# Kernel optimization log

Hardware: AMD Instinct MI355X
Metric: run time of the kernel (lower is better)

## Reference

```python
import jax, jax.numpy as jnp
import numpy as np

H, C, PQ, PV = 12, 16, 4, 8   # heads, c_hidden, qk points, v points
CS, CZ = 384, 128
INF, EPS = 1e5, 1e-8


def quat_to_rot(q):
    w, x, y, z = q[..., 0], q[..., 1], q[..., 2], q[..., 3]
    r = jnp.stack([
        1 - 2 * (y * y + z * z), 2 * (x * y - w * z), 2 * (x * z + w * y),
        2 * (x * y + w * z), 1 - 2 * (x * x + z * z), 2 * (y * z - w * x),
        2 * (x * z - w * y), 2 * (y * z + w * x), 1 - 2 * (x * x + y * y)],
        axis=-1)
    return r.reshape(q.shape[:-1] + (3, 3))


def setup_inputs() -> dict:
    key = jax.random.key(0)
    ks = jax.random.split(key, 20)
    B, N = 1, 768
    s = jax.random.normal(ks[0], (B, N, CS), jnp.float32)
    z = jax.random.normal(ks[1], (B, N, N, CZ), jnp.float32)
    quat = jax.random.normal(ks[2], (B, N, 4), jnp.float32)
    quat = quat / jnp.linalg.norm(quat, axis=-1, keepdims=True)
    rot = quat_to_rot(quat)
    trans = 10.0 * jax.random.normal(ks[3], (B, N, 3), jnp.float32)
    mask = jnp.ones((B, N), jnp.float32)
    ss = jax.random.uniform(ks[4], (B, N, N), jnp.float32)
    sc = 0.02
    W_q = sc * jax.random.normal(ks[5], (CS, H * C), jnp.float32)
    b_q = jnp.zeros((H * C,), jnp.float32)
    W_kv = sc * jax.random.normal(ks[6], (CS, 2 * H * C), jnp.float32)
    b_kv = jnp.zeros((2 * H * C,), jnp.float32)
    W_qp = sc * jax.random.normal(ks[7], (CS, H * PQ * 3), jnp.float32)
    b_qp = jnp.zeros((H * PQ * 3,), jnp.float32)
    W_kvp = sc * jax.random.normal(ks[8], (CS, H * (PQ + PV) * 3), jnp.float32)
    b_kvp = jnp.zeros((H * (PQ + PV) * 3,), jnp.float32)
    W_b = sc * jax.random.normal(ks[9], (CZ, H), jnp.float32)
    b_b = jnp.zeros((H,), jnp.float32)
    head_weights = 0.1 * jax.random.normal(ks[10], (H,), jnp.float32)
    cdim = H * (CZ + C + PV * 4)
    W_out = sc * jax.random.normal(ks[11], (cdim, CS), jnp.float32)
    b_out = jnp.zeros((CS,), jnp.float32)
    return dict(s=s, z=z, rot=rot, trans=trans, mask=mask, ss=ss,
                W_q=W_q, b_q=b_q, W_kv=W_kv, b_kv=b_kv, W_qp=W_qp, b_qp=b_qp,
                W_kvp=W_kvp, b_kvp=b_kvp, W_b=W_b, b_b=b_b,
                head_weights=head_weights, W_out=W_out, b_out=b_out)


def reference(s, z, rot, trans, mask, ss, W_q, b_q, W_kv, b_kv, W_qp, b_qp,
              W_kvp, b_kvp, W_b, b_b, head_weights, W_out, b_out):
    B, N, _ = s.shape
    # scalar q/k/v  [B,N,H,C]
    q = (s @ W_q + b_q).reshape(B, N, H, C)
    kv = (s @ W_kv + b_kv).reshape(B, N, H, 2 * C)
    k, v = kv[..., :C], kv[..., C:]
    # point q/k/v: linear output is [x_all, y_all, z_all] -> stack on last dim
    qp = s @ W_qp + b_qp                                  # [B,N,H*PQ*3]
    qp = jnp.stack(jnp.split(qp, 3, axis=-1), axis=-1)    # [B,N,H*PQ,3] local
    qp = jnp.einsum('bnxy,bnpy->bnpx', rot, qp) + trans[:, :, None]
    qp = qp.reshape(B, N, H, PQ, 3)                       # global frame
    kvp = s @ W_kvp + b_kvp
    kvp = jnp.stack(jnp.split(kvp, 3, axis=-1), axis=-1)  # [B,N,H*(PQ+PV),3]
    kvp = jnp.einsum('bnxy,bnpy->bnpx', rot, kvp) + trans[:, :, None]
    kvp = kvp.reshape(B, N, H, PQ + PV, 3)
    kp, vp = kvp[..., :PQ, :], kvp[..., PQ:, :]
    # scalar attention logits + pair bias
    b = z @ W_b + b_b                                     # [B,N,N,H]
    a = jnp.einsum('bihc,bjhc->bhij', q, k) * np.sqrt(1.0 / (3 * C))
    a = a + np.sqrt(1.0 / 3) * jnp.transpose(b, (0, 3, 1, 2))
    # point-distance attention
    diff = qp[:, :, None] - kp[:, None]                   # [B,N,N,H,PQ,3]
    d2 = jnp.sum(diff * diff, axis=-1)                    # [B,N,N,H,PQ]
    hw = jax.nn.softplus(head_weights) * np.sqrt(1.0 / (3 * (PQ * 9.0 / 2)))
    pt = -0.5 * jnp.sum(d2 * hw[None, None, None, :, None], axis=-1)  # [B,N,N,H]
    a = a + jnp.transpose(pt, (0, 3, 1, 2))
    sq_mask = INF * (mask[:, :, None] * mask[:, None, :] - 1.0)
    a = a + sq_mask[:, None]
    # weighted softmax (ss_usage='multiply', t_ss=1): weights = exp(ss) - 0.99
    weights = jnp.exp(ss) - 0.99                          # [B,N,N]
    e = jnp.exp(a - jnp.max(a, axis=-1, keepdims=True))
    we = e * weights[:, None]
    a = we / jnp.sum(we, axis=-1, keepdims=True)          # [B,H,N,N]
    # outputs
    o = jnp.einsum('bhij,bjhc->bihc', a, v).reshape(B, N, H * C)
    o_pt = jnp.einsum('bhij,bjhpc->bihpc', a, vp)         # [B,N,H,PV,3] global
    o_pt = jnp.einsum('bnyx,bnhpy->bnhpx', rot, o_pt - trans[:, :, None, None])
    o_pt_norm = jnp.sqrt(jnp.sum(o_pt ** 2, axis=-1) + EPS).reshape(B, N, H * PV)
    o_pt = o_pt.reshape(B, N, H * PV, 3)
    o_pair = jnp.einsum('bhij,bijc->bihc', a, z).reshape(B, N, H * CZ)
    cat = jnp.concatenate(
        [o, o_pt[..., 0], o_pt[..., 1], o_pt[..., 2], o_pt_norm, o_pair], axis=-1)
    return cat @ W_out + b_out
```

## Files before the change

### kernel.cpp

```cpp
#include <hip/hip_runtime.h>
#include <math.h>

#define NN 768
#define CSD 384
#define HD 12
#define CD 16
#define PQD 4
#define PVD 8
#define CZD 128
#define CATD 2112

#define OFF_Q      0u
#define OFF_K      147456u
#define OFF_V      294912u
#define OFF_QP     442368u
#define OFF_KP     552960u
#define OFF_VP     663552u
#define OFF_RAW    884736u
#define OFF_B      1327104u
#define OFF_A      8404992u
#define OFF_CAT    15482880u

__device__ __forceinline__ float wcol_val(const float* Wq, const float* Wkv,
                                          const float* Wqp, const float* Wkvp,
                                          int k, int col) {
  if (col < 192) return Wq[k*192 + col];
  if (col < 576) return Wkv[k*384 + (col-192)];
  if (col < 720) return Wqp[k*144 + (col-576)];
  return Wkvp[k*432 + (col-720)];
}
__device__ __forceinline__ float bias_val(const float* bq, const float* bkv,
                                          const float* bqp, const float* bkvp, int col) {
  if (col < 192) return bq[col];
  if (col < 576) return bkv[col-192];
  if (col < 720) return bqp[col-576];
  return bkvp[col-720];
}

__global__ __launch_bounds__(256) void k_proj(const float* __restrict__ s,
    const float* __restrict__ Wq, const float* __restrict__ bq,
    const float* __restrict__ Wkv, const float* __restrict__ bkv,
    const float* __restrict__ Wqp, const float* __restrict__ bqp,
    const float* __restrict__ Wkvp, const float* __restrict__ bkvp,
    float* __restrict__ ws) {
  __shared__ float At[64*17];
  __shared__ float Bt[16*64];
  int t = threadIdx.x;
  int c0 = blockIdx.x * 64;
  int r0 = blockIdx.y * 64;
  float acc[4][4] = {};
  int cc = t & 15, rr = t >> 4;
  for (int kt = 0; kt < CSD; kt += 16) {
    int ka = t & 15, mb = t >> 4;
#pragma unroll
    for (int p = 0; p < 4; ++p) {
      int m = mb + p*16;
      At[m*17 + ka] = s[(r0+m)*CSD + kt + ka];
    }
    int cb = t & 63, kb = t >> 6;
#pragma unroll
    for (int p = 0; p < 4; ++p) {
      int kk = kb + p*4;
      Bt[kk*64 + cb] = wcol_val(Wq,Wkv,Wqp,Wkvp, kt+kk, c0+cb);
    }
    __syncthreads();
#pragma unroll
    for (int k = 0; k < 16; ++k) {
      float a0 = At[(rr*4+0)*17 + k];
      float a1 = At[(rr*4+1)*17 + k];
      float a2 = At[(rr*4+2)*17 + k];
      float a3 = At[(rr*4+3)*17 + k];
      float4 b4 = *(const float4*)&Bt[k*64 + cc*4];
      acc[0][0] = fmaf(a0,b4.x,acc[0][0]); acc[0][1] = fmaf(a0,b4.y,acc[0][1]);
      acc[0][2] = fmaf(a0,b4.z,acc[0][2]); acc[0][3] = fmaf(a0,b4.w,acc[0][3]);
      acc[1][0] = fmaf(a1,b4.x,acc[1][0]); acc[1][1] = fmaf(a1,b4.y,acc[1][1]);
      acc[1][2] = fmaf(a1,b4.z,acc[1][2]); acc[1][3] = fmaf(a1,b4.w,acc[1][3]);
      acc[2][0] = fmaf(a2,b4.x,acc[2][0]); acc[2][1] = fmaf(a2,b4.y,acc[2][1]);
      acc[2][2] = fmaf(a2,b4.z,acc[2][2]); acc[2][3] = fmaf(a2,b4.w,acc[2][3]);
      acc[3][0] = fmaf(a3,b4.x,acc[3][0]); acc[3][1] = fmaf(a3,b4.y,acc[3][1]);
      acc[3][2] = fmaf(a3,b4.z,acc[3][2]); acc[3][3] = fmaf(a3,b4.w,acc[3][3]);
    }
    __syncthreads();
  }
  float* qbuf = ws + OFF_Q; float* kbuf = ws + OFF_K; float* vbuf = ws + OFF_V;
  float* raw  = ws + OFF_RAW;
#pragma unroll
  for (int jj = 0; jj < 4; ++jj) {
    int col = c0 + cc*4 + jj;
    float bv = bias_val(bq,bkv,bqp,bkvp,col);
#pragma unroll
    for (int ii = 0; ii < 4; ++ii) {
      int row = r0 + rr*4 + ii;
      float val = acc[ii][jj] + bv;
      if (col < 192) {
        int h = col >> 4, c = col & 15;
        qbuf[(h*NN + row)*CD + c] = val;
      } else if (col < 576) {
        int u = col - 192; int h = u >> 5; int c2 = u & 31;
        if (c2 < 16) kbuf[(h*NN+row)*CD + c2] = val;
        else         vbuf[(h*NN+row)*CD + (c2-16)] = val;
      } else {
        raw[row*576 + (col-576)] = val;
      }
    }
  }
}

__global__ __launch_bounds__(256) void k_points(const float* __restrict__ rot,
    const float* __restrict__ trans, float* __restrict__ ws) {
  int tg = blockIdx.x*256 + threadIdx.x;
  int n = tg / 192, pidx = tg % 192;
  const float* raw = ws + OFF_RAW + n*576;
  float v0, v1, v2;
  if (pidx < 48) { v0 = raw[pidx]; v1 = raw[48+pidx]; v2 = raw[96+pidx]; }
  else { int pp = pidx-48; v0 = raw[144+pp]; v1 = raw[288+pp]; v2 = raw[432+pp]; }
  const float* R = rot + n*9; const float* T = trans + n*3;
  float g0 = R[0]*v0 + R[1]*v1 + R[2]*v2 + T[0];
  float g1 = R[3]*v0 + R[4]*v1 + R[5]*v2 + T[1];
  float g2 = R[6]*v0 + R[7]*v1 + R[8]*v2 + T[2];
  if (pidx < 48) {
    int h = pidx >> 2, p = pidx & 3;
    float* qp = ws + OFF_QP + ((h*NN + n)*PQD + p)*3;
    qp[0]=g0; qp[1]=g1; qp[2]=g2;
  } else {
    int pp = pidx - 48; int h = pp/12; int q12 = pp - 12*h;
    if (q12 < 4) { float* kp = ws + OFF_KP + ((h*NN+n)*PQD + q12)*3; kp[0]=g0; kp[1]=g1; kp[2]=g2; }
    else         { float* vp = ws + OFF_VP + ((h*NN+n)*PVD + (q12-4))*3; vp[0]=g0; vp[1]=g1; vp[2]=g2; }
  }
}

__global__ __launch_bounds__(256) void k_bias(const float* __restrict__ z,
    const float* __restrict__ Wb, const float* __restrict__ bb, float* __restrict__ ws) {
  __shared__ float wb_sm[CZD*HD];
  __shared__ float bb_sm[HD];
  int t = threadIdx.x;
  for (int idx = t; idx < CZD*HD; idx += 256) wb_sm[idx] = Wb[idx];
  if (t < HD) bb_sm[t] = bb[t];
  __syncthreads();

  int w = t >> 6, lane = t & 63;
  int i = blockIdx.x*4 + w;
  int j = blockIdx.y*64 + lane;
  const float* zrow = z + ((size_t)i*NN + j)*CZD;
  float acc[12];
#pragma unroll
  for (int h = 0; h < 12; ++h) acc[h] = 0.f;

  for (int c0 = 0; c0 < CZD; c0 += 32) {
    float4 zr[8];
#pragma unroll
    for (int u = 0; u < 8; ++u)
      zr[u] = *(const float4*)(zrow + c0 + 4*u);
#pragma unroll
    for (int u = 0; u < 8; ++u) {
#pragma unroll
      for (int cc = 0; cc < 4; ++cc) {
        int c = c0 + 4*u + cc;
        float zv = (cc==0) ? zr[u].x : (cc==1) ? zr[u].y : (cc==2) ? zr[u].z : zr[u].w;
        float4 w0 = *(const float4*)&wb_sm[c*12];
        float4 w1 = *(const float4*)&wb_sm[c*12 + 4];
        float4 w2 = *(const float4*)&wb_sm[c*12 + 8];
        acc[0] = fmaf(zv, w0.x, acc[0]); acc[1] = fmaf(zv, w0.y, acc[1]);
        acc[2] = fmaf(zv, w0.z, acc[2]); acc[3] = fmaf(zv, w0.w, acc[3]);
        acc[4] = fmaf(zv, w1.x, acc[4]); acc[5] = fmaf(zv, w1.y, acc[5]);
        acc[6] = fmaf(zv, w1.z, acc[6]); acc[7] = fmaf(zv, w1.w, acc[7]);
        acc[8] = fmaf(zv, w2.x, acc[8]); acc[9] = fmaf(zv, w2.y, acc[9]);
        acc[10] = fmaf(zv, w2.z, acc[10]); acc[11] = fmaf(zv, w2.w, acc[11]);
      }
    }
  }
  float* bmat = ws + OFF_B;
  const float s2 = 0.57735026918962576f;
#pragma unroll
  for (int h = 0; h < 12; ++h)
    bmat[((size_t)i*HD + h)*NN + j] = s2*(acc[h] + bb_sm[h]);
}

__global__ __launch_bounds__(256) void k_attn(
    const float* __restrict__ mask, const float* __restrict__ ss,
    const float* __restrict__ hwts, float* __restrict__ ws) {
  int h = blockIdx.x, i = blockIdx.y;
  int t = threadIdx.x;
  __shared__ float qsm[16];
  __shared__ float qpsm[12];
  __shared__ float wred[8];
  const float* qbuf = ws + OFF_Q; const float* kbuf = ws + OFF_K;
  const float* qp   = ws + OFF_QP; const float* kp  = ws + OFF_KP;
  const float* bmat = ws + OFF_B;
  float* abuf = ws + OFF_A;
  if (t < 16) qsm[t] = qbuf[(h*NN+i)*CD + t];
  else if (t < 28) qpsm[t-16] = qp[(h*NN+i)*12 + (t-16)];
  __syncthreads();
  float coef = -0.5f * 0.13608276348795434f * log1pf(__expf(hwts[h]));
  float mi = mask[i];
  const float s1 = 0.14433756729740643f;
  float l3[3], ss3[3];
#pragma unroll
  for (int jj = 0; jj < 3; ++jj) {
    int j = t + jj*256;
    const float4* kb = (const float4*)(kbuf + (h*NN+j)*CD);
    float dot = 0.f;
#pragma unroll
    for (int u = 0; u < 4; ++u) {
      float4 kv = kb[u];
      dot = fmaf(qsm[u*4+0], kv.x, dot);
      dot = fmaf(qsm[u*4+1], kv.y, dot);
      dot = fmaf(qsm[u*4+2], kv.z, dot);
      dot = fmaf(qsm[u*4+3], kv.w, dot);
    }
    const float4* kpb = (const float4*)(kp + (h*NN+j)*12);
    float pts = 0.f;
#pragma unroll
    for (int u = 0; u < 3; ++u) {
      float4 kpv = kpb[u];
      float d;
      d = qpsm[u*4+0]-kpv.x; pts = fmaf(d,d,pts);
      d = qpsm[u*4+1]-kpv.y; pts = fmaf(d,d,pts);
      d = qpsm[u*4+2]-kpv.z; pts = fmaf(d,d,pts);
      d = qpsm[u*4+3]-kpv.w; pts = fmaf(d,d,pts);
    }
    float bterm = bmat[((size_t)i*HD + h)*NN + j];
    float lg = fmaf(dot, s1, bterm) + coef*pts + 100000.0f*(mi*mask[j] - 1.0f);
    l3[jj] = lg; ss3[jj] = ss[i*NN + j];
  }
  float mx = fmaxf(l3[0], fmaxf(l3[1], l3[2]));
#pragma unroll
  for (int off = 32; off >= 1; off >>= 1) mx = fmaxf(mx, __shfl_xor(mx, off));
  if ((t & 63) == 0) wred[t>>6] = mx;
  __syncthreads();
  mx = fmaxf(fmaxf(wred[0],wred[1]), fmaxf(wred[2],wred[3]));
  float e3[3]; float sum = 0.f;
#pragma unroll
  for (int jj = 0; jj < 3; ++jj) {
    e3[jj] = __expf(l3[jj]-mx) * (__expf(ss3[jj]) - 0.99f);
    sum += e3[jj];
  }
#pragma unroll
  for (int off = 32; off >= 1; off >>= 1) sum += __shfl_xor(sum, off);
  if ((t & 63) == 0) wred[4 + (t>>6)] = sum;
  __syncthreads();
  sum = (wred[4]+wred[5]) + (wred[6]+wred[7]);
  float inv = 1.0f / sum;
#pragma unroll
  for (int jj = 0; jj < 3; ++jj)
    abuf[((size_t)h*NN + i)*NN + t + jj*256] = e3[jj]*inv;
}

__global__ __launch_bounds__(256) void k_out_v(
    const float* __restrict__ rot, const float* __restrict__ trans, float* __restrict__ ws) {
  int h = blockIdx.x;
  int i = blockIdx.y*4 + (threadIdx.x >> 6);
  int lane = threadIdx.x & 63;
  const float* abuf = ws + OFF_A; const float* vbuf = ws + OFF_V; const float* vpbuf = ws + OFF_VP;
  float* cat = ws + OFF_CAT;
  const float* arow = abuf + ((size_t)h*NN + i)*NN;
  float acc = 0.f;
  if (lane < 40) {
    const float* ptr; int stride;
    if (lane < 16) { ptr = vbuf + (size_t)(h*NN)*CD + lane; stride = CD; }
    else           { ptr = vpbuf + (size_t)(h*NN)*24 + (lane-16); stride = 24; }
    for (int j = 0; j < NN; j += 4) {
      float4 a4 = *(const float4*)(arow + j);
      float x0 = ptr[0];
      float x1 = ptr[stride];
      float x2 = ptr[2*stride];
      float x3 = ptr[3*stride];
      ptr += 4*stride;
      acc = fmaf(a4.x, x0, acc);
      acc = fmaf(a4.y, x1, acc);
      acc = fmaf(a4.z, x2, acc);
      acc = fmaf(a4.w, x3, acc);
    }
  }
  if (lane < 16) {
    cat[(size_t)i*CATD + h*CD + lane] = acc;
  } else if (lane < 40) {
    int pv = lane - 16; int p = pv/3; int x = pv - 3*p;
    int base = 16 + p*3;
    float g0 = __shfl(acc, base+0);
    float g1 = __shfl(acc, base+1);
    float g2 = __shfl(acc, base+2);
    float v0 = g0 - trans[i*3+0];
    float v1 = g1 - trans[i*3+1];
    float v2 = g2 - trans[i*3+2];
    float loc = rot[i*9 + 0*3 + x]*v0 + rot[i*9 + 1*3 + x]*v1 + rot[i*9 + 2*3 + x]*v2;
    cat[(size_t)i*CATD + 192 + x*96 + h*PVD + p] = loc;
    float sq = loc*loc;
    float n2 = __shfl(sq, base+0) + __shfl(sq, base+1) + __shfl(sq, base+2);
    if (x == 0) cat[(size_t)i*CATD + 480 + h*PVD + p] = sqrtf(n2 + 1e-8f);
  }
}

__global__ __launch_bounds__(256) void k_out_pair(const float* __restrict__ z, float* __restrict__ ws) {
  __shared__ float a_sm[HD*NN];
  __shared__ float4 psm[4][HD][32];
  int i = blockIdx.x;
  int t = threadIdx.x;
  const float* abuf = ws + OFF_A;
  float* cat = ws + OFF_CAT;
  for (int h = 0; h < HD; ++h) {
    if (t < 192)
      *(float4*)&a_sm[h*NN + t*4] = *(const float4*)(abuf + ((size_t)h*NN + i)*NN + t*4);
  }
  __syncthreads();
  int c4 = t & 31, jc = t >> 5;
  const float* zbase = z + ((size_t)i*NN + (size_t)jc*96)*CZD + c4*4;
  float4 acc[12];
#pragma unroll
  for (int h = 0; h < 12; ++h) acc[h] = make_float4(0.f,0.f,0.f,0.f);
  for (int jj = 0; jj < 96; jj += 4) {
    float4 z0 = *(const float4*)(zbase + (size_t)(jj+0)*CZD);
    float4 z1 = *(const float4*)(zbase + (size_t)(jj+1)*CZD);
    float4 z2 = *(const float4*)(zbase + (size_t)(jj+2)*CZD);
    float4 z3 = *(const float4*)(zbase + (size_t)(jj+3)*CZD);
    int j0 = jc*96 + jj;
#pragma unroll
    for (int h = 0; h < 12; ++h) {
      float4 av = *(const float4*)&a_sm[h*NN + j0];
      acc[h].x = fmaf(av.x, z0.x, acc[h].x); acc[h].y = fmaf(av.x, z0.y, acc[h].y);
      acc[h].z = fmaf(av.x, z0.z, acc[h].z); acc[h].w = fmaf(av.x, z0.w, acc[h].w);
      acc[h].x = fmaf(av.y, z1.x, acc[h].x); acc[h].y = fmaf(av.y, z1.y, acc[h].y);
      acc[h].z = fmaf(av.y, z1.z, acc[h].z); acc[h].w = fmaf(av.y, z1.w, acc[h].w);
      acc[h].x = fmaf(av.z, z2.x, acc[h].x); acc[h].y = fmaf(av.z, z2.y, acc[h].y);
      acc[h].z = fmaf(av.z, z2.z, acc[h].z); acc[h].w = fmaf(av.z, z2.w, acc[h].w);
      acc[h].x = fmaf(av.w, z3.x, acc[h].x); acc[h].y = fmaf(av.w, z3.y, acc[h].y);
      acc[h].z = fmaf(av.w, z3.z, acc[h].z); acc[h].w = fmaf(av.w, z3.w, acc[h].w);
    }
  }
  int wv = t >> 6, ln = t & 63;
#pragma unroll
  for (int h = 0; h < 12; ++h) {
    acc[h].x += __shfl_down(acc[h].x, 32);
    acc[h].y += __shfl_down(acc[h].y, 32);
    acc[h].z += __shfl_down(acc[h].z, 32);
    acc[h].w += __shfl_down(acc[h].w, 32);
  }
  if (ln < 32) {
#pragma unroll
    for (int h = 0; h < 12; ++h) psm[wv][h][ln] = acc[h];
  }
  __syncthreads();
  for (int o = t; o < 384; o += 256) {
    int h = o >> 5, cc = o & 31;
    float4 s0 = psm[0][h][cc], s1 = psm[1][h][cc], s2 = psm[2][h][cc], s3 = psm[3][h][cc];
    float4 r;
    r.x = (s0.x+s1.x)+(s2.x+s3.x);
    r.y = (s0.y+s1.y)+(s2.y+s3.y);
    r.z = (s0.z+s1.z)+(s2.z+s3.z);
    r.w = (s0.w+s1.w)+(s2.w+s3.w);
    *(float4*)&cat[(size_t)i*CATD + 576 + h*CZD + cc*4] = r;
  }
}

__global__ __launch_bounds__(256) void k_init_out(const float* __restrict__ bout, float* __restrict__ out) {
  int idx = blockIdx.x*256 + threadIdx.x;
  if (idx < NN*CSD) out[idx] = bout[idx % CSD];
}

__global__ __launch_bounds__(256) void k_final(const float* __restrict__ Wout,
    float* __restrict__ out, const float* __restrict__ ws) {
  __shared__ float At[64*17];
  __shared__ float Bt[16*64];
  const float* cat = ws + OFF_CAT;
  int t = threadIdx.x;
  int c0 = blockIdx.x*64, r0 = blockIdx.y*64;
  int kstart = blockIdx.z*528;
  float acc[4][4] = {};
  int cc = t & 15, rr = t >> 4;
  for (int kt = 0; kt < 528; kt += 16) {
    int ka = t & 15, mb = t >> 4;
#pragma unroll
    for (int p = 0; p < 4; ++p) {
      int m = mb + p*16;
      At[m*17 + ka] = cat[(size_t)(r0+m)*CATD + kstart + kt + ka];
    }
    int cb = t & 63, kb = t >> 6;
#pragma unroll
    for (int p = 0; p < 4; ++p) {
      int kk = kb + p*4;
      Bt[kk*64 + cb] = Wout[(size_t)(kstart+kt+kk)*CSD + c0 + cb];
    }
    __syncthreads();
#pragma unroll
    for (int k = 0; k < 16; ++k) {
      float a0 = At[(rr*4+0)*17 + k];
      float a1 = At[(rr*4+1)*17 + k];
      float a2 = At[(rr*4+2)*17 + k];
      float a3 = At[(rr*4+3)*17 + k];
      float4 b4 = *(const float4*)&Bt[k*64 + cc*4];
      acc[0][0] = fmaf(a0,b4.x,acc[0][0]); acc[0][1] = fmaf(a0,b4.y,acc[0][1]);
      acc[0][2] = fmaf(a0,b4.z,acc[0][2]); acc[0][3] = fmaf(a0,b4.w,acc[0][3]);
      acc[1][0] = fmaf(a1,b4.x,acc[1][0]); acc[1][1] = fmaf(a1,b4.y,acc[1][1]);
      acc[1][2] = fmaf(a1,b4.z,acc[1][2]); acc[1][3] = fmaf(a1,b4.w,acc[1][3]);
      acc[2][0] = fmaf(a2,b4.x,acc[2][0]); acc[2][1] = fmaf(a2,b4.y,acc[2][1]);
      acc[2][2] = fmaf(a2,b4.z,acc[2][2]); acc[2][3] = fmaf(a2,b4.w,acc[2][3]);
      acc[3][0] = fmaf(a3,b4.x,acc[3][0]); acc[3][1] = fmaf(a3,b4.y,acc[3][1]);
      acc[3][2] = fmaf(a3,b4.z,acc[3][2]); acc[3][3] = fmaf(a3,b4.w,acc[3][3]);
    }
    __syncthreads();
  }
#pragma unroll
  for (int ii = 0; ii < 4; ++ii)
#pragma unroll
    for (int jj = 0; jj < 4; ++jj)
      atomicAdd(&out[(size_t)(r0+rr*4+ii)*CSD + c0 + cc*4 + jj], acc[ii][jj]);
}

extern "C" void kernel_launch(void* const* d_in, const int* in_sizes, int n_in,
                              void* d_out, int out_size, void* d_ws, size_t ws_size,
                              hipStream_t stream) {
  const float* s    = (const float*)d_in[0];
  const float* z    = (const float*)d_in[1];
  const float* rot  = (const float*)d_in[2];
  const float* trans= (const float*)d_in[3];
  const float* mask = (const float*)d_in[4];
  const float* ss   = (const float*)d_in[5];
  const float* Wq   = (const float*)d_in[6];
  const float* bq   = (const float*)d_in[7];
  const float* Wkv  = (const float*)d_in[8];
  const float* bkv  = (const float*)d_in[9];
  const float* Wqp  = (const float*)d_in[10];
  const float* bqp  = (const float*)d_in[11];
  const float* Wkvp = (const float*)d_in[12];
  const float* bkvp = (const float*)d_in[13];
  const float* Wb   = (const float*)d_in[14];
  const float* bb   = (const float*)d_in[15];
  const float* hw   = (const float*)d_in[16];
  const float* Wout = (const float*)d_in[17];
  const float* bout = (const float*)d_in[18];
  float* ws  = (float*)d_ws;
  float* out = (float*)d_out;

  hipLaunchKernelGGL(k_proj, dim3(18,12), dim3(256), 0, stream,
                     s, Wq,bq, Wkv,bkv, Wqp,bqp, Wkvp,bkvp, ws);
  hipLaunchKernelGGL(k_points, dim3(576), dim3(256), 0, stream, rot, trans, ws);
  hipLaunchKernelGGL(k_bias, dim3(192,12), dim3(256), 0, stream, z, Wb, bb, ws);
  hipLaunchKernelGGL(k_attn, dim3(12,768), dim3(256), 0, stream, mask, ss, hw, ws);
  hipLaunchKernelGGL(k_out_v, dim3(12,192), dim3(256), 0, stream, rot, trans, ws);
  hipLaunchKernelGGL(k_out_pair, dim3(768), dim3(256), 0, stream, z, ws);
  hipLaunchKernelGGL(k_init_out, dim3(1152), dim3(256), 0, stream, bout, out);
  hipLaunchKernelGGL(k_final, dim3(6,12,4), dim3(256), 0, stream, Wout, out, ws);
}
```

Measured before the change: 859.8 us.

## Restructure pair-bias kernel for coalesced z reads with register weights and shuffles

The z·W_b bias projection is rewritten so that 16 lanes share one (i,j) row and each lane reads a contiguous 8-channel slice. Previously each thread streamed a whole 512-byte row, which coalesces poorly. Each lane keeps its 8×12 slice of W_b in registers instead of shared memory, reduces partial sums across lanes with xor shuffles, and prefetches the next z slice one step ahead. In exchange it adds shuffle work and register pressure, and only one lane in sixteen does the scattered stores.

```diff
diff --git a/kernel.cpp b/kernel.cpp
--- a/kernel.cpp
+++ b/kernel.cpp
@@ -131,49 +131,61 @@
 
 __global__ __launch_bounds__(256) void k_bias(const float* __restrict__ z,
     const float* __restrict__ Wb, const float* __restrict__ bb, float* __restrict__ ws) {
-  __shared__ float wb_sm[CZD*HD];
-  __shared__ float bb_sm[HD];
   int t = threadIdx.x;
-  for (int idx = t; idx < CZD*HD; idx += 256) wb_sm[idx] = Wb[idx];
-  if (t < HD) bb_sm[t] = bb[t];
-  __syncthreads();
-
-  int w = t >> 6, lane = t & 63;
-  int i = blockIdx.x*4 + w;
-  int j = blockIdx.y*64 + lane;
-  const float* zrow = z + ((size_t)i*NN + j)*CZD;
-  float acc[12];
-#pragma unroll
-  for (int h = 0; h < 12; ++h) acc[h] = 0.f;
-
-  for (int c0 = 0; c0 < CZD; c0 += 32) {
-    float4 zr[8];
-#pragma unroll
-    for (int u = 0; u < 8; ++u)
-      zr[u] = *(const float4*)(zrow + c0 + 4*u);
-#pragma unroll
-    for (int u = 0; u < 8; ++u) {
-#pragma unroll
-      for (int cc = 0; cc < 4; ++cc) {
-        int c = c0 + 4*u + cc;
-        float zv = (cc==0) ? zr[u].x : (cc==1) ? zr[u].y : (cc==2) ? zr[u].z : zr[u].w;
-        float4 w0 = *(const float4*)&wb_sm[c*12];
-        float4 w1 = *(const float4*)&wb_sm[c*12 + 4];
-        float4 w2 = *(const float4*)&wb_sm[c*12 + 8];
-        acc[0] = fmaf(zv, w0.x, acc[0]); acc[1] = fmaf(zv, w0.y, acc[1]);
-        acc[2] = fmaf(zv, w0.z, acc[2]); acc[3] = fmaf(zv, w0.w, acc[3]);
-        acc[4] = fmaf(zv, w1.x, acc[4]); acc[5] = fmaf(zv, w1.y, acc[5]);
-        acc[6] = fmaf(zv, w1.z, acc[6]); acc[7] = fmaf(zv, w1.w, acc[7]);
-        acc[8] = fmaf(zv, w2.x, acc[8]); acc[9] = fmaf(zv, w2.y, acc[9]);
-        acc[10] = fmaf(zv, w2.z, acc[10]); acc[11] = fmaf(zv, w2.w, acc[11]);
-      }
-    }
-  }
+  int q = t & 15, g = t >> 4;
+  float wbr[8][12];
+#pragma unroll
+  for (int cc = 0; cc < 8; ++cc) {
+    const float* wp = Wb + (q*8 + cc)*HD;
+#pragma unroll
+    for (int h = 0; h < 12; ++h) wbr[cc][h] = wp[h];
+  }
+  float bbr[12];
+#pragma unroll
+  for (int h = 0; h < 12; ++h) bbr[h] = bb[h];
+
+  const int base = blockIdx.x * 512;
+  const float* zq = z + (size_t)(base + g)*CZD + q*8;
+  float4 p0a = *(const float4*)(zq);
+  float4 p0b = *(const float4*)(zq + 4);
+  float4 p1a = *(const float4*)(zq + 16*CZD);
+  float4 p1b = *(const float4*)(zq + 16*CZD + 4);
   float* bmat = ws + OFF_B;
   const float s2 = 0.57735026918962576f;
-#pragma unroll
-  for (int h = 0; h < 12; ++h)
-    bmat[((size_t)i*HD + h)*NN + j] = s2*(acc[h] + bb_sm[h]);
+  for (int s = 0; s < 32; ++s) {
+    float4 za = p0a, zb = p0b;
+    p0a = p1a; p0b = p1b;
+    if (s < 30) {
+      p1a = *(const float4*)(zq + (size_t)(s+2)*16*CZD);
+      p1b = *(const float4*)(zq + (size_t)(s+2)*16*CZD + 4);
+    }
+    float acc[12];
+#pragma unroll
+    for (int h = 0; h < 12; ++h) acc[h] = 0.f;
+#pragma unroll
+    for (int h = 0; h < 12; ++h) {
+      acc[h] = fmaf(za.x, wbr[0][h], acc[h]);
+      acc[h] = fmaf(za.y, wbr[1][h], acc[h]);
+      acc[h] = fmaf(za.z, wbr[2][h], acc[h]);
+      acc[h] = fmaf(za.w, wbr[3][h], acc[h]);
+      acc[h] = fmaf(zb.x, wbr[4][h], acc[h]);
+      acc[h] = fmaf(zb.y, wbr[5][h], acc[h]);
+      acc[h] = fmaf(zb.z, wbr[6][h], acc[h]);
+      acc[h] = fmaf(zb.w, wbr[7][h], acc[h]);
+    }
+#pragma unroll
+    for (int off = 8; off >= 1; off >>= 1)
+#pragma unroll
+      for (int h = 0; h < 12; ++h) acc[h] += __shfl_xor(acc[h], off);
+    if (q == 0) {
+      int r = base + g + 16*s;
+      int i = r / NN;
+      int j = r - i*NN;
+#pragma unroll
+      for (int h = 0; h < 12; ++h)
+        bmat[((size_t)i*HD + h)*NN + j] = s2*(acc[h] + bbr[h]);
+    }
+  }
 }
 
 __global__ __launch_bounds__(256) void k_attn(
@@ -434,7 +446,7 @@
   hipLaunchKernelGGL(k_proj, dim3(18,12), dim3(256), 0, stream,
                      s, Wq,bq, Wkv,bkv, Wqp,bqp, Wkvp,bkvp, ws);
   hipLaunchKernelGGL(k_points, dim3(576), dim3(256), 0, stream, rot, trans, ws);
-  hipLaunchKernelGGL(k_bias, dim3(192,12), dim3(256), 0, stream, z, Wb, bb, ws);
+  hipLaunchKernelGGL(k_bias, dim3(1152), dim3(256), 0, stream, z, Wb, bb, ws);
   hipLaunchKernelGGL(k_attn, dim3(12,768), dim3(256), 0, stream, mask, ss, hw, ws);
   hipLaunchKernelGGL(k_out_v, dim3(12,192), dim3(256), 0, stream, rot, trans, ws);
   hipLaunchKernelGGL(k_out_pair, dim3(768), dim3(256), 0, stream, z, ws);
```

New measurement: 849.2 us. Within noise of the previous version (-1.2%).

## Restructure pair-bias projection so lanes split channels with shuffle reduction

Applied to the files above, without the earlier changes.

The z-to-bias projection now assigns 32 lanes to one pair row, each lane loading a contiguous float4 of channels so global reads are fully coalesced. Previously each thread streamed its own 512-byte row. Each lane keeps its slice of W_b in registers, and a butterfly of xor-shuffles both reduces and distributes the 12 head sums across lanes. The grid becomes a 1D persistent-style launch of 1024 blocks with a two-deep prefetch of z. The cost is extra shuffle instructions and scattered bias stores, where only some lanes write.

```diff
diff --git a/kernel.cpp b/kernel.cpp
--- a/kernel.cpp
+++ b/kernel.cpp
@@ -131,49 +131,70 @@
 
 __global__ __launch_bounds__(256) void k_bias(const float* __restrict__ z,
     const float* __restrict__ Wb, const float* __restrict__ bb, float* __restrict__ ws) {
-  __shared__ float wb_sm[CZD*HD];
-  __shared__ float bb_sm[HD];
   int t = threadIdx.x;
-  for (int idx = t; idx < CZD*HD; idx += 256) wb_sm[idx] = Wb[idx];
-  if (t < HD) bb_sm[t] = bb[t];
-  __syncthreads();
-
-  int w = t >> 6, lane = t & 63;
-  int i = blockIdx.x*4 + w;
-  int j = blockIdx.y*64 + lane;
-  const float* zrow = z + ((size_t)i*NN + j)*CZD;
-  float acc[12];
-#pragma unroll
-  for (int h = 0; h < 12; ++h) acc[h] = 0.f;
-
-  for (int c0 = 0; c0 < CZD; c0 += 32) {
-    float4 zr[8];
-#pragma unroll
-    for (int u = 0; u < 8; ++u)
-      zr[u] = *(const float4*)(zrow + c0 + 4*u);
-#pragma unroll
-    for (int u = 0; u < 8; ++u) {
-#pragma unroll
-      for (int cc = 0; cc < 4; ++cc) {
-        int c = c0 + 4*u + cc;
-        float zv = (cc==0) ? zr[u].x : (cc==1) ? zr[u].y : (cc==2) ? zr[u].z : zr[u].w;
-        float4 w0 = *(const float4*)&wb_sm[c*12];
-        float4 w1 = *(const float4*)&wb_sm[c*12 + 4];
-        float4 w2 = *(const float4*)&wb_sm[c*12 + 8];
-        acc[0] = fmaf(zv, w0.x, acc[0]); acc[1] = fmaf(zv, w0.y, acc[1]);
-        acc[2] = fmaf(zv, w0.z, acc[2]); acc[3] = fmaf(zv, w0.w, acc[3]);
-        acc[4] = fmaf(zv, w1.x, acc[4]); acc[5] = fmaf(zv, w1.y, acc[5]);
-        acc[6] = fmaf(zv, w1.z, acc[6]); acc[7] = fmaf(zv, w1.w, acc[7]);
-        acc[8] = fmaf(zv, w2.x, acc[8]); acc[9] = fmaf(zv, w2.y, acc[9]);
-        acc[10] = fmaf(zv, w2.z, acc[10]); acc[11] = fmaf(zv, w2.w, acc[11]);
-      }
-    }
-  }
+  int q = t & 31;
+  int rs = t >> 5;
+  float wbr[4][12];
+#pragma unroll
+  for (int cc = 0; cc < 4; ++cc) {
+    const float* wp = Wb + (q*4 + cc)*HD;
+#pragma unroll
+    for (int h = 0; h < 12; ++h) wbr[cc][h] = wp[h];
+  }
+  const int b4 = (q>>4)&1, b3 = (q>>3)&1, b2 = (q>>2)&1, b1 = (q>>1)&1, b0 = q&1;
+  const int hmine = 6*b4 + 3*b3 + (b2 ? 2 : b1);
+  const bool writer = (b0 == 0) && (b2 == 0 || b1 == 0);
+  const float bbh = bb[hmine];
+
+  const int base = blockIdx.x * 576;
+  const float* zp = z + (size_t)(base + rs)*CZD + q*4;
+  float4 p0 = *(const float4*)(zp);
+  float4 p1 = *(const float4*)(zp + 8*CZD);
   float* bmat = ws + OFF_B;
   const float s2 = 0.57735026918962576f;
-#pragma unroll
-  for (int h = 0; h < 12; ++h)
-    bmat[((size_t)i*HD + h)*NN + j] = s2*(acc[h] + bb_sm[h]);
+  for (int s = 0; s < 72; ++s) {
+    float4 za = p0; p0 = p1;
+    if (s < 70) p1 = *(const float4*)(zp + (size_t)(s+2)*8*CZD);
+    float acc[12];
+#pragma unroll
+    for (int h = 0; h < 12; ++h) {
+      float a = za.x * wbr[0][h];
+      a = fmaf(za.y, wbr[1][h], a);
+      a = fmaf(za.z, wbr[2][h], a);
+      a = fmaf(za.w, wbr[3][h], a);
+      acc[h] = a;
+    }
+    float na[6];
+#pragma unroll
+    for (int m = 0; m < 6; ++m) {
+      float keep = b4 ? acc[m+6] : acc[m];
+      float give = b4 ? acc[m]   : acc[m+6];
+      na[m] = keep + __shfl_xor(give, 16);
+    }
+    float nb[3];
+#pragma unroll
+    for (int m = 0; m < 3; ++m) {
+      float keep = b3 ? na[m+3] : na[m];
+      float give = b3 ? na[m]   : na[m+3];
+      nb[m] = keep + __shfl_xor(give, 8);
+    }
+    float k0 = b2 ? nb[2] : nb[0];
+    float g0v = b2 ? nb[0] : nb[2];
+    float k1 = b2 ? 0.f   : nb[1];
+    float g1v = b2 ? nb[1] : 0.f;
+    float c0v = k0 + __shfl_xor(g0v, 4);
+    float c1v = k1 + __shfl_xor(g1v, 4);
+    float k2 = b2 ? c0v : (b1 ? c1v : c0v);
+    float g2v = b2 ? c0v : (b1 ? c0v : c1v);
+    float d0 = k2 + __shfl_xor(g2v, 2);
+    float e0 = d0 + __shfl_xor(d0, 1);
+    if (writer) {
+      int r = base + 8*s + rs;
+      int i = r / NN;
+      int j = r - i*NN;
+      bmat[((size_t)i*HD + hmine)*NN + j] = s2*(e0 + bbh);
+    }
+  }
 }
 
 __global__ __launch_bounds__(256) void k_attn(
@@ -434,7 +455,7 @@
   hipLaunchKernelGGL(k_proj, dim3(18,12), dim3(256), 0, stream,
                      s, Wq,bq, Wkv,bkv, Wqp,bqp, Wkvp,bkvp, ws);
   hipLaunchKernelGGL(k_points, dim3(576), dim3(256), 0, stream, rot, trans, ws);
-  hipLaunchKernelGGL(k_bias, dim3(192,12), dim3(256), 0, stream, z, Wb, bb, ws);
+  hipLaunchKernelGGL(k_bias, dim3(1024), dim3(256), 0, stream, z, Wb, bb, ws);
   hipLaunchKernelGGL(k_attn, dim3(12,768), dim3(256), 0, stream, mask, ss, hw, ws);
   hipLaunchKernelGGL(k_out_v, dim3(12,192), dim3(256), 0, stream, rot, trans, ws);
   hipLaunchKernelGGL(k_out_pair, dim3(768), dim3(256), 0, stream, z, ws);
```

Result: faster. 829.1 us (-3.6%).
